# Optimization experiments

Hardware: AMD Instinct MI355X
Metric: run time of the kernel (lower is better)

Reference implementation:

```python
import jax, jax.numpy as jnp
import numpy as np

EPS = 1e-5
GROUPS = 384

def _dwconv(x, w, stride, pad):
    # x: [N,C,H,W], w: [O, C/groups, kh, kw] (depthwise: C/groups == 1)
    return jax.lax.conv_general_dilated(
        x, w,
        window_strides=(stride, stride),
        padding=[(pad, pad), (pad, pad)],
        dimension_numbers=('NCHW', 'OIHW', 'NCHW'),
        feature_group_count=GROUPS,
    )

def _bn(y, gamma, beta):
    # training-mode BatchNorm2d: batch statistics over (N,H,W)
    mean = jnp.mean(y, axis=(0, 2, 3), keepdims=True)
    var = jnp.var(y, axis=(0, 2, 3), keepdims=True)
    g = gamma[None, :, None, None]
    b = beta[None, :, None, None]
    return (y - mean) * jax.lax.rsqrt(var + EPS) * g + b

def setup_inputs() -> dict:
    key = jax.random.key(0)
    k1, k2, k3 = jax.random.split(key, 3)
    C = 384
    x = jax.random.normal(k1, (32, C, 64, 64), dtype=jnp.float32)
    w_lk = jax.random.normal(k2, (C, 1, 7, 7), dtype=jnp.float32) * 0.05
    w_sk = jax.random.normal(k3, (C, 1, 3, 3), dtype=jnp.float32) * 0.1
    gamma_lk = jnp.ones((C,), jnp.float32)
    beta_lk = jnp.zeros((C,), jnp.float32)
    gamma_sk = jnp.ones((C,), jnp.float32)
    beta_sk = jnp.zeros((C,), jnp.float32)
    return {"x": x, "w_lk": w_lk, "gamma_lk": gamma_lk, "beta_lk": beta_lk,
            "w_sk": w_sk, "gamma_sk": gamma_sk, "beta_sk": beta_sk}

def reference(x, w_lk, gamma_lk, beta_lk, w_sk, gamma_sk, beta_sk):
    stride = 2
    # large-kernel depthwise branch: conv7x7 (pad 3) + BN
    out = _bn(_dwconv(x, w_lk, stride, 3), gamma_lk, beta_lk)
    # small-kernel depthwise branch: conv3x3 (pad 1) + BN, added in
    out = out + _bn(_dwconv(x, w_sk, stride, 1), gamma_sk, beta_sk)
    # exact (erf) GELU, matching torch nn.GELU() default
    return jax.nn.gelu(out, approximate=False)
```

## Files before the change

kernel.cpp:

```cpp
#include <hip/hip_runtime.h>
#include <hip/hip_fp16.h>
#include <cmath>

#define NB 32
#define CH 384
#define IH 64
#define IW 64
#define OH 32
#define OW 32
#define PR 70
#define PWQ 18

typedef unsigned int u32x4 __attribute__((ext_vector_type(4)));
typedef float        f32x4 __attribute__((ext_vector_type(4)));

__global__ __launch_bounds__(128, 4) void conv_stats_kernel(
    const float* __restrict__ x,
    const float* __restrict__ w_lk,
    const float* __restrict__ w_sk,
    uint2* __restrict__ yls,
    float* __restrict__ partial)
{
    __shared__ float sxq[4][PR][PWQ];

    const int nc  = blockIdx.x;
    const int n   = nc / CH;
    const int c   = nc % CH;
    const int tid = threadIdx.x;

    const float4* xp4 = (const float4*)(x + (size_t)nc * (IH * IW));
    float4 vbuf[8];
#pragma unroll
    for (int it = 0; it < 8; ++it) vbuf[it] = xp4[tid + it * 128];

    for (int i = tid; i < 4 * 3 * PWQ; i += 128) {
        const int f = i / (3 * PWQ);
        const int rem = i % (3 * PWQ);
        const int r = rem / PWQ, q = rem % PWQ;
        sxq[f][r][q] = 0.0f;
        sxq[f][67 + r][q] = 0.0f;
    }
    for (int i = tid; i < 64 * 6; i += 128) {
        const int r = 3 + i / 6;
        const int t = i % 6;
        const int f = (t < 3) ? t : ((t == 3) ? 3 : t - 4);
        const int q = (t < 3) ? 0 : ((t == 3) ? 16 : 17);
        sxq[f][r][q] = 0.0f;
    }

#pragma unroll
    for (int it = 0; it < 8; ++it) {
        const int i = tid + it * 128;
        const float4 v = vbuf[it];
        const int r  = (i >> 4) + 3;
        const int q4 = i & 15;
        sxq[3][r][q4]     = v.x;
        sxq[0][r][q4 + 1] = v.y;
        sxq[1][r][q4 + 1] = v.z;
        sxq[2][r][q4 + 1] = v.w;
    }
    __syncthreads();

    float wl[49], ws9[9];
#pragma unroll
    for (int t = 0; t < 49; ++t) wl[t] = w_lk[c * 49 + t];
#pragma unroll
    for (int t = 0; t < 9; ++t)  ws9[t] = w_sk[c * 9 + t];

    const int lane = tid & 63;
    const int wv   = tid >> 6;
    const int j16  = lane & 15;
    const int g    = lane >> 4;
    const int qb   = j16;
    const int oy0  = (wv * 4 + g) * 4;
    const int prb  = 2 * oy0;

    float alA[4] = {0.f,0.f,0.f,0.f}, alB[4] = {0.f,0.f,0.f,0.f};
    float asA[4] = {0.f,0.f,0.f,0.f}, asB[4] = {0.f,0.f,0.f,0.f};

#pragma unroll
    for (int k = 0; k < 13; ++k) {
        const int pr = prb + k;
        const float E0 = sxq[0][pr][qb];
        const float E1 = sxq[0][pr][qb + 1];
        const float E2 = sxq[0][pr][qb + 2];
        const float F0 = sxq[1][pr][qb];
        const float F1 = sxq[1][pr][qb + 1];
        const float G0 = sxq[2][pr][qb];
        const float G1 = sxq[2][pr][qb + 1];
        const float H0 = sxq[3][pr][qb];
        const float H1 = sxq[3][pr][qb + 1];
#pragma unroll
        for (int j = 0; j < 4; ++j) {
            if (k >= 2 * j && k <= 2 * j + 6) {
                const int ky = k - 2 * j;
                alA[j] = fmaf(E0, wl[ky * 7 + 0], alA[j]);
                alA[j] = fmaf(F0, wl[ky * 7 + 1], alA[j]);
                alA[j] = fmaf(G0, wl[ky * 7 + 2], alA[j]);
                alA[j] = fmaf(H0, wl[ky * 7 + 3], alA[j]);
                alA[j] = fmaf(E1, wl[ky * 7 + 4], alA[j]);
                alA[j] = fmaf(F1, wl[ky * 7 + 5], alA[j]);
                alA[j] = fmaf(G1, wl[ky * 7 + 6], alA[j]);
                alB[j] = fmaf(G0, wl[ky * 7 + 0], alB[j]);
                alB[j] = fmaf(H0, wl[ky * 7 + 1], alB[j]);
                alB[j] = fmaf(E1, wl[ky * 7 + 2], alB[j]);
                alB[j] = fmaf(F1, wl[ky * 7 + 3], alB[j]);
                alB[j] = fmaf(G1, wl[ky * 7 + 4], alB[j]);
                alB[j] = fmaf(H1, wl[ky * 7 + 5], alB[j]);
                alB[j] = fmaf(E2, wl[ky * 7 + 6], alB[j]);
            }
            if (k >= 2 * j + 2 && k <= 2 * j + 4) {
                const int kys = k - 2 * j - 2;
                asA[j] = fmaf(G0, ws9[kys * 3 + 0], asA[j]);
                asA[j] = fmaf(H0, ws9[kys * 3 + 1], asA[j]);
                asA[j] = fmaf(E1, ws9[kys * 3 + 2], asA[j]);
                asB[j] = fmaf(E1, ws9[kys * 3 + 0], asB[j]);
                asB[j] = fmaf(F1, ws9[kys * 3 + 1], asB[j]);
                asB[j] = fmaf(G1, ws9[kys * 3 + 2], asB[j]);
            }
        }
    }

    float s0 = 0.f, s1 = 0.f, s2 = 0.f, s3 = 0.f;
    uint2* yp = yls + (size_t)nc * (OH * OW / 2);
#pragma unroll
    for (int j = 0; j < 4; ++j) {
        const int oy = oy0 + j;
        const __half2 hA = __floats2half2_rn(alA[j], asA[j]);
        const __half2 hB = __floats2half2_rn(alB[j], asB[j]);
        uint2 u;
        u.x = *reinterpret_cast<const unsigned int*>(&hA);
        u.y = *reinterpret_cast<const unsigned int*>(&hB);
        yp[oy * (OW / 2) + j16] = u;
        s0 += alA[j] + alB[j];
        s1 += alA[j] * alA[j] + alB[j] * alB[j];
        s2 += asA[j] + asB[j];
        s3 += asA[j] * asA[j] + asB[j] * asB[j];
    }

#pragma unroll
    for (int off = 32; off >= 1; off >>= 1) {
        s0 += __shfl_down(s0, off);
        s1 += __shfl_down(s1, off);
        s2 += __shfl_down(s2, off);
        s3 += __shfl_down(s3, off);
    }
    if (lane == 0) {
        ((float4*)partial)[(c * NB + n) * 2 + wv] = make_float4(s0, s1, s2, s3);
    }
}

__global__ __launch_bounds__(256) void apply_kernel(
    const u32x4* __restrict__ yls4,
    const float* __restrict__ partial,
    const float* __restrict__ gamma_lk, const float* __restrict__ beta_lk,
    const float* __restrict__ gamma_sk, const float* __restrict__ beta_sk,
    f32x4* __restrict__ out)
{
    __shared__ float sp[4];

    const int b = blockIdx.x;
    const int c = b % CH;
    const int tid = threadIdx.x;

    if (tid < 64) {
        float4 v = ((const float4*)partial)[c * 64 + tid];
        float s0 = v.x, s1 = v.y, s2 = v.z, s3 = v.w;
#pragma unroll
        for (int off = 32; off >= 1; off >>= 1) {
            s0 += __shfl_down(s0, off);
            s1 += __shfl_down(s1, off);
            s2 += __shfl_down(s2, off);
            s3 += __shfl_down(s3, off);
        }
        if (tid == 0) {
            const float inv_cnt = 1.0f / (float)(NB * OH * OW);
            const float mean_l = s0 * inv_cnt;
            const float var_l  = s1 * inv_cnt - mean_l * mean_l;
            const float sc_l   = gamma_lk[c] * rsqrtf(var_l + 1e-5f);
            const float sh_l   = beta_lk[c] - mean_l * sc_l;
            const float mean_s = s2 * inv_cnt;
            const float var_s  = s3 * inv_cnt - mean_s * mean_s;
            const float sc_s   = gamma_sk[c] * rsqrtf(var_s + 1e-5f);
            const float sh_s   = beta_sk[c] - mean_s * sc_s;
            sp[0] = sc_l; sp[1] = sh_l; sp[2] = sc_s; sp[3] = sh_s;
        }
    }
    __syncthreads();

    const float sc_l = sp[0], sh_l = sp[1], sc_s = sp[2], sh_s = sp[3];

    const int i = b * 256 + tid;
    const u32x4 v = __builtin_nontemporal_load(yls4 + i);
    const unsigned int uv0 = v.x, uv1 = v.y, uv2 = v.z, uv3 = v.w;
    const __half2 h0 = *reinterpret_cast<const __half2*>(&uv0);
    const __half2 h1 = *reinterpret_cast<const __half2*>(&uv1);
    const __half2 h2 = *reinterpret_cast<const __half2*>(&uv2);
    const __half2 h3 = *reinterpret_cast<const __half2*>(&uv3);

    const float v0 = fmaf(__low2float(h0), sc_l, sh_l) + fmaf(__high2float(h0), sc_s, sh_s);
    const float v1 = fmaf(__low2float(h1), sc_l, sh_l) + fmaf(__high2float(h1), sc_s, sh_s);
    const float v2 = fmaf(__low2float(h2), sc_l, sh_l) + fmaf(__high2float(h2), sc_s, sh_s);
    const float v3 = fmaf(__low2float(h3), sc_l, sh_l) + fmaf(__high2float(h3), sc_s, sh_s);

    f32x4 r;
    r.x = 0.5f * v0 * (1.0f + erff(v0 * 0.70710678118654752f));
    r.y = 0.5f * v1 * (1.0f + erff(v1 * 0.70710678118654752f));
    r.z = 0.5f * v2 * (1.0f + erff(v2 * 0.70710678118654752f));
    r.w = 0.5f * v3 * (1.0f + erff(v3 * 0.70710678118654752f));
    __builtin_nontemporal_store(r, out + i);
}

extern "C" void kernel_launch(void* const* d_in, const int* in_sizes, int n_in,
                              void* d_out, int out_size, void* d_ws, size_t ws_size,
                              hipStream_t stream) {
    const float* x        = (const float*)d_in[0];
    const float* w_lk     = (const float*)d_in[1];
    const float* gamma_lk = (const float*)d_in[2];
    const float* beta_lk  = (const float*)d_in[3];
    const float* w_sk     = (const float*)d_in[4];
    const float* gamma_sk = (const float*)d_in[5];
    const float* beta_sk  = (const float*)d_in[6];
    float* out = (float*)d_out;

    float* partial = (float*)d_ws;
    uint2* yls     = (uint2*)(partial + CH * NB * 2 * 4);

    conv_stats_kernel<<<NB * CH, 128, 0, stream>>>(x, w_lk, w_sk, yls, partial);
    apply_kernel<<<NB * CH, 256, 0, stream>>>(
        (const u32x4*)yls, partial, gamma_lk, beta_lk, gamma_sk, beta_sk,
        (f32x4*)out);
}
```

Before: 60.79 us.

## Stage input as packed fp16 pairs and use dot2 for depthwise convs

```diff
diff --git a/kernel.cpp b/kernel.cpp
--- a/kernel.cpp
+++ b/kernel.cpp
@@ -9,19 +9,28 @@
 #define OH 32
 #define OW 32
 #define PR 70
-#define PWQ 18
-
+#define SP 35
+
+typedef _Float16     h2    __attribute__((ext_vector_type(2)));
 typedef unsigned int u32x4 __attribute__((ext_vector_type(4)));
 typedef float        f32x4 __attribute__((ext_vector_type(4)));
+
+__device__ __forceinline__ float fdot2(h2 a, h2 b, float c) {
+#if __has_builtin(__builtin_amdgcn_fdot2)
+    return __builtin_amdgcn_fdot2(a, b, c, false);
+#else
+    return c + (float)a.x * (float)b.x + (float)a.y * (float)b.y;
+#endif
+}
 
 __global__ __launch_bounds__(128, 4) void conv_stats_kernel(
     const float* __restrict__ x,
     const float* __restrict__ w_lk,
     const float* __restrict__ w_sk,
-    uint2* __restrict__ yls,
+    unsigned int* __restrict__ yls,
     float* __restrict__ partial)
 {
-    __shared__ float sxq[4][PR][PWQ];
+    __shared__ h2 sx[PR][SP];
 
     const int nc  = blockIdx.x;
     const int n   = nc / CH;
@@ -33,19 +42,16 @@
 #pragma unroll
     for (int it = 0; it < 8; ++it) vbuf[it] = xp4[tid + it * 128];
 
-    for (int i = tid; i < 4 * 3 * PWQ; i += 128) {
-        const int f = i / (3 * PWQ);
-        const int rem = i % (3 * PWQ);
-        const int r = rem / PWQ, q = rem % PWQ;
-        sxq[f][r][q] = 0.0f;
-        sxq[f][67 + r][q] = 0.0f;
-    }
-    for (int i = tid; i < 64 * 6; i += 128) {
-        const int r = 3 + i / 6;
-        const int t = i % 6;
-        const int f = (t < 3) ? t : ((t == 3) ? 3 : t - 4);
-        const int q = (t < 3) ? 0 : ((t == 3) ? 16 : 17);
-        sxq[f][r][q] = 0.0f;
+    h2 z2; z2.x = (_Float16)0.f; z2.y = (_Float16)0.f;
+
+    for (int i = tid; i < 5 * SP; i += 128) {
+        const int r = i / SP, q = i % SP;
+        sx[(r < 3) ? r : (64 + r)][q] = z2;
+    }
+    for (int i = tid; i < 64 * 3; i += 128) {
+        const int r = 3 + i / 3;
+        const int t = i % 3;
+        sx[r][(t < 2) ? t : 34] = z2;
     }
 
 #pragma unroll
@@ -54,88 +60,80 @@
         const float4 v = vbuf[it];
         const int r  = (i >> 4) + 3;
         const int q4 = i & 15;
-        sxq[3][r][q4]     = v.x;
-        sxq[0][r][q4 + 1] = v.y;
-        sxq[1][r][q4 + 1] = v.z;
-        sxq[2][r][q4 + 1] = v.w;
+        h2 a, b;
+        a.x = (_Float16)v.x; a.y = (_Float16)v.y;
+        b.x = (_Float16)v.z; b.y = (_Float16)v.w;
+        sx[r][2 * q4 + 2] = a;
+        sx[r][2 * q4 + 3] = b;
     }
     __syncthreads();
 
-    float wl[49], ws9[9];
-#pragma unroll
-    for (int t = 0; t < 49; ++t) wl[t] = w_lk[c * 49 + t];
-#pragma unroll
-    for (int t = 0; t < 9; ++t)  ws9[t] = w_sk[c * 9 + t];
+    h2 pw[7][4];
+#pragma unroll
+    for (int ky = 0; ky < 7; ++ky) {
+        const float w0 = w_lk[c * 49 + ky * 7 + 0];
+        const float w1 = w_lk[c * 49 + ky * 7 + 1];
+        const float w2 = w_lk[c * 49 + ky * 7 + 2];
+        const float w3 = w_lk[c * 49 + ky * 7 + 3];
+        const float w4 = w_lk[c * 49 + ky * 7 + 4];
+        const float w5 = w_lk[c * 49 + ky * 7 + 5];
+        const float w6 = w_lk[c * 49 + ky * 7 + 6];
+        pw[ky][0].x = (_Float16)0.f; pw[ky][0].y = (_Float16)w0;
+        pw[ky][1].x = (_Float16)w1;  pw[ky][1].y = (_Float16)w2;
+        pw[ky][2].x = (_Float16)w3;  pw[ky][2].y = (_Float16)w4;
+        pw[ky][3].x = (_Float16)w5;  pw[ky][3].y = (_Float16)w6;
+    }
+    h2 sw[3][2];
+#pragma unroll
+    for (int ks = 0; ks < 3; ++ks) {
+        const float s0 = w_sk[c * 9 + ks * 3 + 0];
+        const float s1 = w_sk[c * 9 + ks * 3 + 1];
+        const float s2 = w_sk[c * 9 + ks * 3 + 2];
+        sw[ks][0].x = (_Float16)0.f; sw[ks][0].y = (_Float16)s0;
+        sw[ks][1].x = (_Float16)s1;  sw[ks][1].y = (_Float16)s2;
+    }
 
     const int lane = tid & 63;
     const int wv   = tid >> 6;
-    const int j16  = lane & 15;
-    const int g    = lane >> 4;
-    const int qb   = j16;
-    const int oy0  = (wv * 4 + g) * 4;
-    const int prb  = 2 * oy0;
-
-    float alA[4] = {0.f,0.f,0.f,0.f}, alB[4] = {0.f,0.f,0.f,0.f};
-    float asA[4] = {0.f,0.f,0.f,0.f}, asB[4] = {0.f,0.f,0.f,0.f};
-
-#pragma unroll
-    for (int k = 0; k < 13; ++k) {
-        const int pr = prb + k;
-        const float E0 = sxq[0][pr][qb];
-        const float E1 = sxq[0][pr][qb + 1];
-        const float E2 = sxq[0][pr][qb + 2];
-        const float F0 = sxq[1][pr][qb];
-        const float F1 = sxq[1][pr][qb + 1];
-        const float G0 = sxq[2][pr][qb];
-        const float G1 = sxq[2][pr][qb + 1];
-        const float H0 = sxq[3][pr][qb];
-        const float H1 = sxq[3][pr][qb + 1];
-#pragma unroll
-        for (int j = 0; j < 4; ++j) {
+    const int ox   = lane & 31;
+    const int g1   = lane >> 5;
+    const int r8   = g1 + 2 * wv;
+    const int pr0  = 16 * r8;
+
+    float accl[8] = {0.f,0.f,0.f,0.f,0.f,0.f,0.f,0.f};
+    float accs[8] = {0.f,0.f,0.f,0.f,0.f,0.f,0.f,0.f};
+
+#pragma unroll
+    for (int k = 0; k <= 20; ++k) {
+        const h2 L0 = sx[pr0 + k][ox];
+        const h2 L1 = sx[pr0 + k][ox + 1];
+        const h2 L2 = sx[pr0 + k][ox + 2];
+        const h2 L3 = sx[pr0 + k][ox + 3];
+#pragma unroll
+        for (int j = 0; j < 8; ++j) {
             if (k >= 2 * j && k <= 2 * j + 6) {
                 const int ky = k - 2 * j;
-                alA[j] = fmaf(E0, wl[ky * 7 + 0], alA[j]);
-                alA[j] = fmaf(F0, wl[ky * 7 + 1], alA[j]);
-                alA[j] = fmaf(G0, wl[ky * 7 + 2], alA[j]);
-                alA[j] = fmaf(H0, wl[ky * 7 + 3], alA[j]);
-                alA[j] = fmaf(E1, wl[ky * 7 + 4], alA[j]);
-                alA[j] = fmaf(F1, wl[ky * 7 + 5], alA[j]);
-                alA[j] = fmaf(G1, wl[ky * 7 + 6], alA[j]);
-                alB[j] = fmaf(G0, wl[ky * 7 + 0], alB[j]);
-                alB[j] = fmaf(H0, wl[ky * 7 + 1], alB[j]);
-                alB[j] = fmaf(E1, wl[ky * 7 + 2], alB[j]);
-                alB[j] = fmaf(F1, wl[ky * 7 + 3], alB[j]);
-                alB[j] = fmaf(G1, wl[ky * 7 + 4], alB[j]);
-                alB[j] = fmaf(H1, wl[ky * 7 + 5], alB[j]);
-                alB[j] = fmaf(E2, wl[ky * 7 + 6], alB[j]);
+                accl[j] = fdot2(L0, pw[ky][0], accl[j]);
+                accl[j] = fdot2(L1, pw[ky][1], accl[j]);
+                accl[j] = fdot2(L2, pw[ky][2], accl[j]);
+                accl[j] = fdot2(L3, pw[ky][3], accl[j]);
             }
             if (k >= 2 * j + 2 && k <= 2 * j + 4) {
-                const int kys = k - 2 * j - 2;
-                asA[j] = fmaf(G0, ws9[kys * 3 + 0], asA[j]);
-                asA[j] = fmaf(H0, ws9[kys * 3 + 1], asA[j]);
-                asA[j] = fmaf(E1, ws9[kys * 3 + 2], asA[j]);
-                asB[j] = fmaf(E1, ws9[kys * 3 + 0], asB[j]);
-                asB[j] = fmaf(F1, ws9[kys * 3 + 1], asB[j]);
-                asB[j] = fmaf(G1, ws9[kys * 3 + 2], asB[j]);
+                const int ks = k - 2 * j - 2;
+                accs[j] = fdot2(L1, sw[ks][0], accs[j]);
+                accs[j] = fdot2(L2, sw[ks][1], accs[j]);
             }
         }
     }
 
     float s0 = 0.f, s1 = 0.f, s2 = 0.f, s3 = 0.f;
-    uint2* yp = yls + (size_t)nc * (OH * OW / 2);
-#pragma unroll
-    for (int j = 0; j < 4; ++j) {
-        const int oy = oy0 + j;
-        const __half2 hA = __floats2half2_rn(alA[j], asA[j]);
-        const __half2 hB = __floats2half2_rn(alB[j], asB[j]);
-        uint2 u;
-        u.x = *reinterpret_cast<const unsigned int*>(&hA);
-        u.y = *reinterpret_cast<const unsigned int*>(&hB);
-        yp[oy * (OW / 2) + j16] = u;
-        s0 += alA[j] + alB[j];
-        s1 += alA[j] * alA[j] + alB[j] * alB[j];
-        s2 += asA[j] + asB[j];
-        s3 += asA[j] * asA[j] + asB[j] * asB[j];
+    unsigned int* yp = yls + (size_t)nc * (OH * OW);
+#pragma unroll
+    for (int j = 0; j < 8; ++j) {
+        const __half2 h = __floats2half2_rn(accl[j], accs[j]);
+        yp[(8 * r8 + j) * OW + ox] = *reinterpret_cast<const unsigned int*>(&h);
+        s0 += accl[j]; s1 += accl[j] * accl[j];
+        s2 += accs[j]; s3 += accs[j] * accs[j];
     }
 
 #pragma unroll
@@ -195,12 +193,12 @@
     const unsigned int uv0 = v.x, uv1 = v.y, uv2 = v.z, uv3 = v.w;
     const __half2 h0 = *reinterpret_cast<const __half2*>(&uv0);
     const __half2 h1 = *reinterpret_cast<const __half2*>(&uv1);
-    const __half2 h2 = *reinterpret_cast<const __half2*>(&uv2);
+    const __half2 h2v = *reinterpret_cast<const __half2*>(&uv2);
     const __half2 h3 = *reinterpret_cast<const __half2*>(&uv3);
 
     const float v0 = fmaf(__low2float(h0), sc_l, sh_l) + fmaf(__high2float(h0), sc_s, sh_s);
     const float v1 = fmaf(__low2float(h1), sc_l, sh_l) + fmaf(__high2float(h1), sc_s, sh_s);
-    const float v2 = fmaf(__low2float(h2), sc_l, sh_l) + fmaf(__high2float(h2), sc_s, sh_s);
+    const float v2 = fmaf(__low2float(h2v), sc_l, sh_l) + fmaf(__high2float(h2v), sc_s, sh_s);
     const float v3 = fmaf(__low2float(h3), sc_l, sh_l) + fmaf(__high2float(h3), sc_s, sh_s);
 
     f32x4 r;
@@ -223,8 +221,8 @@
     const float* beta_sk  = (const float*)d_in[6];
     float* out = (float*)d_out;
 
-    float* partial = (float*)d_ws;
-    uint2* yls     = (uint2*)(partial + CH * NB * 2 * 4);
+    float*        partial = (float*)d_ws;
+    unsigned int* yls     = (unsigned int*)(partial + CH * NB * 2 * 4);
 
     conv_stats_kernel<<<NB * CH, 128, 0, stream>>>(x, w_lk, w_sk, yls, partial);
     apply_kernel<<<NB * CH, 256, 0, stream>>>(
```

New measurement: 64.60 us. 6.3% more time.
